# Optimization experiments

Hardware: AMD Instinct MI355X
Metric: run time of the kernel (lower is better)

## Reference

```python
import jax, jax.numpy as jnp
import numpy as np

N_NODES = 50000
N_EDGES = 800000
IN_CH = 256
OUT_CH = 64
HEADS = 4
NEG_SLOPE = 0.2


def setup_inputs() -> dict:
    key = jax.random.key(0)
    k = jax.random.split(key, 7)
    x = jax.random.normal(k[0], (N_NODES, IN_CH), dtype=jnp.float32)
    edge_index = jax.random.randint(k[1], (2, N_EDGES), 0, N_NODES, dtype=jnp.int32)
    # Glorot-style init for the linear projection and attention vectors
    W = jax.random.normal(k[2], (IN_CH, HEADS * OUT_CH), dtype=jnp.float32) / np.sqrt(IN_CH)
    att_src = jax.random.normal(k[3], (HEADS, OUT_CH), dtype=jnp.float32) / np.sqrt(OUT_CH)
    att_dst = jax.random.normal(k[4], (HEADS, OUT_CH), dtype=jnp.float32) / np.sqrt(OUT_CH)
    bias = jnp.zeros((HEADS * OUT_CH,), dtype=jnp.float32)
    return {"x": x, "edge_index": edge_index, "W": W,
            "att_src": att_src, "att_dst": att_dst, "bias": bias}


def reference(x, edge_index, W, att_src, att_dst, bias):
    N = x.shape[0]
    # PyG GATConv default: add self-loops
    loop = jnp.arange(N, dtype=edge_index.dtype)
    src = jnp.concatenate([edge_index[0], loop])
    dst = jnp.concatenate([edge_index[1], loop])

    h = (x @ W).reshape(N, HEADS, OUT_CH)          # [N,H,C]
    a_src = jnp.einsum('nhc,hc->nh', h, att_src)    # [N,H]
    a_dst = jnp.einsum('nhc,hc->nh', h, att_dst)    # [N,H]

    alpha = a_src[src] + a_dst[dst]                 # [E,H]
    alpha = jax.nn.leaky_relu(alpha, NEG_SLOPE)

    # segment softmax over edges grouped by destination node
    amax = jax.ops.segment_max(alpha, dst, num_segments=N)
    amax = jnp.where(jnp.isfinite(amax), amax, 0.0)
    e = jnp.exp(alpha - amax[dst])
    denom = jax.ops.segment_sum(e, dst, num_segments=N)
    coef = e / (denom[dst] + 1e-16)                 # [E,H]

    msg = coef[..., None] * h[src]                  # [E,H,C]
    out = jax.ops.segment_sum(msg, dst, num_segments=N)  # [N,H,C]
    out = out.reshape(N, HEADS * OUT_CH) + bias
    return jax.nn.relu(out)
```

## Files before the change

### kernel.cpp

```cpp
#include <hip/hip_runtime.h>
#include <hip/hip_bf16.h>

#define HC 256
#define NEG_SLOPE 0.2f
#define LDA 264

typedef short short8_t __attribute__((ext_vector_type(8)));
typedef float float4_t __attribute__((ext_vector_type(4)));

__device__ __forceinline__ unsigned short f2bf(float f) {
  unsigned u = __float_as_uint(f);
  return (unsigned short)((u + 0x7fffu + ((u >> 16) & 1u)) >> 16);
}
__device__ __forceinline__ float bf2f(unsigned short b) {
  return __uint_as_float(((unsigned)b) << 16);
}

__global__ void wt_deg(const float* __restrict__ W, unsigned short* __restrict__ Wt,
                       const int* __restrict__ ei, int* __restrict__ deg, int E)
{
  if (blockIdx.x < 256) {
    const int k = blockIdx.x;
    const int n = threadIdx.x;
    Wt[n * 256 + k] = f2bf(W[k * 256 + n]);
    return;
  }
  const int base = ((blockIdx.x - 256) * 256 + threadIdx.x) * 4;
  if (base + 3 < E) {
    const int4 d4 = *(const int4*)&ei[E + base];
    atomicAdd(&deg[d4.x], 1);
    atomicAdd(&deg[d4.y], 1);
    atomicAdd(&deg[d4.z], 1);
    atomicAdd(&deg[d4.w], 1);
  } else {
    for (int e = base; e < E; ++e) atomicAdd(&deg[ei[E + e]], 1);
  }
}

__global__ __launch_bounds__(256) void gemm_mfma(
    const float* __restrict__ x, const unsigned short* __restrict__ Wt,
    const float* __restrict__ att_src, const float* __restrict__ att_dst,
    unsigned short* __restrict__ h, float* __restrict__ a_src,
    float* __restrict__ a_dst, int nnodes)
{
  __shared__ unsigned short As[64 * LDA];
  const int t    = threadIdx.x;
  const int wv   = t >> 6;
  const int lane = t & 63;
  const int r0   = blockIdx.x * 64;

  {
    const int row = t >> 2;
    const int kc  = (t & 3) * 64;
    const int gr  = r0 + row;
    unsigned pk[32];
    if (gr < nnodes) {
      const float4* p = (const float4*)(x + (size_t)gr * 256 + kc);
      #pragma unroll
      for (int i = 0; i < 16; ++i) {
        const float4 v = p[i];
        __hip_bfloat162 b0 = __float22bfloat162_rn(make_float2(v.x, v.y));
        __hip_bfloat162 b1 = __float22bfloat162_rn(make_float2(v.z, v.w));
        pk[2 * i]     = *(unsigned*)&b0;
        pk[2 * i + 1] = *(unsigned*)&b1;
      }
    } else {
      #pragma unroll
      for (int i = 0; i < 32; ++i) pk[i] = 0;
    }
    uint4* d = (uint4*)&As[row * LDA + kc];
    #pragma unroll
    for (int i = 0; i < 8; ++i)
      d[i] = make_uint4(pk[4 * i], pk[4 * i + 1], pk[4 * i + 2], pk[4 * i + 3]);
  }
  __syncthreads();

  const int q = lane >> 4, l15 = lane & 15;
  float4_t acc[4][4] = {};

  #pragma unroll
  for (int ks = 0; ks < 8; ++ks) {
    const int ko = ks * 32 + q * 8;
    short8_t bfr[4], af[4];
    #pragma unroll
    for (int nt = 0; nt < 4; ++nt)
      bfr[nt] = *(const short8_t*)&Wt[(size_t)(64 * wv + 16 * nt + l15) * 256 + ko];
    #pragma unroll
    for (int mt = 0; mt < 4; ++mt)
      af[mt] = *(const short8_t*)&As[(16 * mt + l15) * LDA + ko];
    #pragma unroll
    for (int mt = 0; mt < 4; ++mt)
      #pragma unroll
      for (int nt = 0; nt < 4; ++nt)
        acc[mt][nt] = __builtin_amdgcn_mfma_f32_16x16x32_bf16(
            af[mt], bfr[nt], acc[mt][nt], 0, 0, 0);
  }

  float atts[4], attd[4];
  #pragma unroll
  for (int nt = 0; nt < 4; ++nt) {
    atts[nt] = att_src[wv * 64 + 16 * nt + l15];
    attd[nt] = att_dst[wv * 64 + 16 * nt + l15];
  }

  #pragma unroll
  for (int mt = 0; mt < 4; ++mt) {
    #pragma unroll
    for (int reg = 0; reg < 4; ++reg) {
      const int row = r0 + 16 * mt + 4 * q + reg;
      const bool ok = row < nnodes;
      float ps = 0.f, pd = 0.f;
      #pragma unroll
      for (int nt = 0; nt < 4; ++nt) {
        const float v = acc[mt][nt][reg];
        if (ok) h[(size_t)row * 256 + 64 * wv + 16 * nt + l15] = f2bf(v);
        ps += v * atts[nt];
        pd += v * attd[nt];
      }
      #pragma unroll
      for (int off = 8; off; off >>= 1) {
        ps += __shfl_down(ps, off, 16);
        pd += __shfl_down(pd, off, 16);
      }
      if (ok && l15 == 0) {
        a_src[row * 4 + wv] = ps;
        a_dst[row * 4 + wv] = pd;
      }
    }
  }
}

__global__ __launch_bounds__(256) void scan_p1(const int* __restrict__ deg,
                                               int* __restrict__ bsum, int n)
{
  __shared__ int ws[4];
  const int t = threadIdx.x, lane = t & 63, wv = t >> 6;
  const int base = blockIdx.x * 1024 + t * 4;
  int4 v = make_int4(0, 0, 0, 0);
  if (base + 3 < n) v = *(const int4*)&deg[base];
  else {
    if (base + 0 < n) v.x = deg[base + 0];
    if (base + 1 < n) v.y = deg[base + 1];
    if (base + 2 < n) v.z = deg[base + 2];
  }
  int s = (v.x + v.y) + (v.z + v.w);
  #pragma unroll
  for (int off = 32; off; off >>= 1) s += __shfl_down(s, off, 64);
  if (lane == 0) ws[wv] = s;
  __syncthreads();
  if (t == 0) bsum[blockIdx.x] = (ws[0] + ws[1]) + (ws[2] + ws[3]);
}

__global__ __launch_bounds__(1024) void scan_p2(const int* __restrict__ bsum,
                                                int* __restrict__ boff,
                                                int* __restrict__ rowptr,
                                                int nb, int n)
{
  __shared__ int wsum[16], woff[16];
  const int t = threadIdx.x, lane = t & 63, wv = t >> 6;
  int v = (t < nb) ? bsum[t] : 0;
  int sc = v;
  #pragma unroll
  for (int off = 1; off < 64; off <<= 1) {
    int u = __shfl_up(sc, off, 64);
    if (lane >= off) sc += u;
  }
  if (lane == 63) wsum[wv] = sc;
  __syncthreads();
  if (t == 0) {
    int run = 0;
    #pragma unroll
    for (int i = 0; i < 16; ++i) { int x = wsum[i]; woff[i] = run; run += x; }
    rowptr[n] = run;
  }
  __syncthreads();
  if (t < nb) boff[t] = woff[wv] + sc - v;
}

__global__ __launch_bounds__(256) void scan_p3(const int* __restrict__ deg,
                                               const int* __restrict__ boff,
                                               int* __restrict__ rowptr,
                                               int* __restrict__ cursor, int n)
{
  __shared__ int wsum[4], woff[4];
  const int t = threadIdx.x, lane = t & 63, wv = t >> 6;
  const int base = blockIdx.x * 1024 + t * 4;
  int4 v = make_int4(0, 0, 0, 0);
  if (base + 3 < n) v = *(const int4*)&deg[base];
  else {
    if (base + 0 < n) v.x = deg[base + 0];
    if (base + 1 < n) v.y = deg[base + 1];
    if (base + 2 < n) v.z = deg[base + 2];
  }
  const int s = (v.x + v.y) + (v.z + v.w);
  int sc = s;
  #pragma unroll
  for (int off = 1; off < 64; off <<= 1) {
    int u = __shfl_up(sc, off, 64);
    if (lane >= off) sc += u;
  }
  if (lane == 63) wsum[wv] = sc;
  __syncthreads();
  if (t == 0) {
    int run = 0;
    #pragma unroll
    for (int i = 0; i < 4; ++i) { int x = wsum[i]; woff[i] = run; run += x; }
  }
  __syncthreads();
  int excl = boff[blockIdx.x] + woff[wv] + (sc - s);
  int4 r;
  r.x = excl;
  r.y = r.x + v.x;
  r.z = r.y + v.y;
  r.w = r.z + v.z;
  if (base + 3 < n) {
    *(int4*)&rowptr[base] = r;
    *(int4*)&cursor[base] = r;
  } else {
    if (base + 0 < n) { rowptr[base + 0] = r.x; cursor[base + 0] = r.x; }
    if (base + 1 < n) { rowptr[base + 1] = r.y; cursor[base + 1] = r.y; }
    if (base + 2 < n) { rowptr[base + 2] = r.z; cursor[base + 2] = r.z; }
  }
}

__device__ __forceinline__ void fill_one(
    int s, int d, int dlo, int dhi, const float* __restrict__ a_src,
    const float* __restrict__ a_dst, int* __restrict__ cursor,
    int* __restrict__ csr_src, float4* __restrict__ wexp)
{
  if (d < dlo || d >= dhi) return;
  const int pos = atomicAdd(&cursor[d], 1);
  csr_src[pos] = s;
  const float4 as = ((const float4*)a_src)[s];
  const float4 ad = ((const float4*)a_dst)[d];
  float4 al;
  al.x = as.x + ad.x; al.y = as.y + ad.y;
  al.z = as.z + ad.z; al.w = as.w + ad.w;
  al.x = al.x > 0.f ? al.x : NEG_SLOPE * al.x;
  al.y = al.y > 0.f ? al.y : NEG_SLOPE * al.y;
  al.z = al.z > 0.f ? al.z : NEG_SLOPE * al.z;
  al.w = al.w > 0.f ? al.w : NEG_SLOPE * al.w;
  al.x = expf(al.x); al.y = expf(al.y); al.z = expf(al.z); al.w = expf(al.w);
  wexp[pos] = al;
}

__global__ __launch_bounds__(256) void fill_csr(
    const int* __restrict__ ei, const float* __restrict__ a_src,
    const float* __restrict__ a_dst, int* __restrict__ cursor,
    int* __restrict__ csr_src, float4* __restrict__ wexp, int E, int nnodes)
{
  const int g    = blockIdx.x & 7;
  const int bg   = blockIdx.x >> 3;
  const int nbg  = gridDim.x >> 3;
  const int gsz  = (nnodes + 7) >> 3;
  const int dlo  = g * gsz;
  const int dhi  = min(dlo + gsz, nnodes);
  const int E4   = E >> 2;

  for (int c = bg * 256 + threadIdx.x; c < E4; c += nbg * 256) {
    const int4 d4 = *(const int4*)&ei[E + 4 * c];
    const int4 s4 = *(const int4*)&ei[4 * c];
    fill_one(s4.x, d4.x, dlo, dhi, a_src, a_dst, cursor, csr_src, wexp);
    fill_one(s4.y, d4.y, dlo, dhi, a_src, a_dst, cursor, csr_src, wexp);
    fill_one(s4.z, d4.z, dlo, dhi, a_src, a_dst, cursor, csr_src, wexp);
    fill_one(s4.w, d4.w, dlo, dhi, a_src, a_dst, cursor, csr_src, wexp);
  }
  for (int e = E4 * 4 + bg * 256 + threadIdx.x; e < E; e += nbg * 256)
    fill_one(ei[e], ei[E + e], dlo, dhi, a_src, a_dst, cursor, csr_src, wexp);
}

__device__ __forceinline__ float4 ld_h(const unsigned short* __restrict__ h,
                                       int row, int cb)
{
  const ushort4 u = *(const ushort4*)&h[(size_t)row * 256 + cb];
  return make_float4(bf2f(u.x), bf2f(u.y), bf2f(u.z), bf2f(u.w));
}

__global__ __launch_bounds__(256) void gather_kernel(
    const int* __restrict__ rowptr, const int* __restrict__ csr_src,
    const float* __restrict__ wexp, const unsigned short* __restrict__ h,
    const float* __restrict__ a_src, const float* __restrict__ a_dst,
    const float* __restrict__ bias, float* __restrict__ out, int n)
{
  const int per8 = gridDim.x >> 3;
  const int vb   = (blockIdx.x & 7) * per8 + (blockIdx.x >> 3);
  const int wave = threadIdx.x >> 6;
  const int lane = threadIdx.x & 63;
  const int d = vb * 4 + wave;
  if (d >= n) return;

  const int head = lane >> 4;
  const int cb   = lane * 4;

  float alpha = a_src[d * 4 + head] + a_dst[d * 4 + head];
  alpha = alpha > 0.f ? alpha : NEG_SLOPE * alpha;
  float w = expf(alpha);
  float dsum = w;
  float4 hv = ld_h(h, d, cb);
  float4 acc = make_float4(w * hv.x, w * hv.y, w * hv.z, w * hv.w);

  int j = rowptr[d];
  const int end = rowptr[d + 1];

  for (; j + 7 < end; j += 8) {
    const int4 sa = *(const int4*)&csr_src[j];
    const int4 sb = *(const int4*)&csr_src[j + 4];
    float wj[8];
    #pragma unroll
    for (int k = 0; k < 8; ++k) wj[k] = wexp[(j + k) * 4 + head];
    const float4 h0 = ld_h(h, sa.x, cb);
    const float4 h1 = ld_h(h, sa.y, cb);
    const float4 h2 = ld_h(h, sa.z, cb);
    const float4 h3 = ld_h(h, sa.w, cb);
    const float4 h4 = ld_h(h, sb.x, cb);
    const float4 h5 = ld_h(h, sb.y, cb);
    const float4 h6 = ld_h(h, sb.z, cb);
    const float4 h7 = ld_h(h, sb.w, cb);
    dsum += ((wj[0] + wj[1]) + (wj[2] + wj[3])) + ((wj[4] + wj[5]) + (wj[6] + wj[7]));
    acc.x += wj[0] * h0.x + wj[1] * h1.x + wj[2] * h2.x + wj[3] * h3.x
           + wj[4] * h4.x + wj[5] * h5.x + wj[6] * h6.x + wj[7] * h7.x;
    acc.y += wj[0] * h0.y + wj[1] * h1.y + wj[2] * h2.y + wj[3] * h3.y
           + wj[4] * h4.y + wj[5] * h5.y + wj[6] * h6.y + wj[7] * h7.y;
    acc.z += wj[0] * h0.z + wj[1] * h1.z + wj[2] * h2.z + wj[3] * h3.z
           + wj[4] * h4.z + wj[5] * h5.z + wj[6] * h6.z + wj[7] * h7.z;
    acc.w += wj[0] * h0.w + wj[1] * h1.w + wj[2] * h2.w + wj[3] * h3.w
           + wj[4] * h4.w + wj[5] * h5.w + wj[6] * h6.w + wj[7] * h7.w;
  }
  for (; j < end; ++j) {
    const int s0 = csr_src[j];
    const float w0 = wexp[j * 4 + head];
    const float4 h0 = ld_h(h, s0, cb);
    dsum += w0;
    acc.x += w0 * h0.x; acc.y += w0 * h0.y;
    acc.z += w0 * h0.z; acc.w += w0 * h0.w;
  }

  const float inv = 1.f / (dsum + 1e-16f);
  const float4 b4 = ((const float4*)bias)[lane];
  float4 o;
  o.x = acc.x * inv + b4.x; o.x = o.x > 0.f ? o.x : 0.f;
  o.y = acc.y * inv + b4.y; o.y = o.y > 0.f ? o.y : 0.f;
  o.z = acc.z * inv + b4.z; o.z = o.z > 0.f ? o.z : 0.f;
  o.w = acc.w * inv + b4.w; o.w = o.w > 0.f ? o.w : 0.f;
  *(float4*)&out[(size_t)d * 256 + cb] = o;
}

extern "C" void kernel_launch(void* const* d_in, const int* in_sizes, int n_in,
                              void* d_out, int out_size, void* d_ws, size_t ws_size,
                              hipStream_t stream)
{
  const float* x       = (const float*)d_in[0];
  const int*   ei      = (const int*)d_in[1];
  const float* W       = (const float*)d_in[2];
  const float* att_src = (const float*)d_in[3];
  const float* att_dst = (const float*)d_in[4];
  const float* bias    = (const float*)d_in[5];

  const int nnodes = in_sizes[0] / HC;
  const int E      = in_sizes[1] / 2;
  const int nb     = (nnodes + 1023) / 1024;
  const int degBlocks    = (E + 1023) / 1024;
  const int gemmBlocks   = (nnodes + 63) / 64;
  const int gatherBlocks = (((nnodes + 3) / 4) + 7) & ~7;

  float* out = (float*)d_out;
  char* ws = (char*)d_ws;
  unsigned short* h  = (unsigned short*)ws;
  float* a_src = (float*)(ws + (size_t)nnodes * HC * 2);
  float* a_dst = a_src + (size_t)nnodes * 4;
  unsigned short* Wt = (unsigned short*)(a_dst + (size_t)nnodes * 4);
  int* deg    = (int*)((char*)Wt + 256 * 256 * 2);
  int* rowptr = deg + nnodes;
  int* cursor = rowptr + ((nnodes + 1 + 3) & ~3);
  int* bsum   = cursor + nnodes;
  int* boff   = bsum + ((nb + 3) & ~3);
  float4* wexp = (float4*)(boff + ((nb + 3) & ~3));
  int* csr    = (int*)(wexp + E);

  hipMemsetAsync(deg, 0, (size_t)nnodes * sizeof(int), stream);

  wt_deg<<<256 + degBlocks, 256, 0, stream>>>(W, Wt, ei, deg, E);

  gemm_mfma<<<gemmBlocks, 256, 0, stream>>>(
      x, Wt, att_src, att_dst, h, a_src, a_dst, nnodes);

  scan_p1<<<nb, 256, 0, stream>>>(deg, bsum, nnodes);
  scan_p2<<<1, 1024, 0, stream>>>(bsum, boff, rowptr, nb, nnodes);
  scan_p3<<<nb, 256, 0, stream>>>(deg, boff, rowptr, cursor, nnodes);

  fill_csr<<<1024, 256, 0, stream>>>(ei, a_src, a_dst, cursor, csr,
                                     (float4*)wexp, E, nnodes);

  gather_kernel<<<gatherBlocks, 256, 0, stream>>>(
      rowptr, csr, (const float*)wexp, h, a_src, a_dst, bias, out, nnodes);
}
```

Measured before the change: 282.7 us.

## Pack CSR source and bf16 edge weights into one record; transpose GEMM epilogue

Edge source index and the four exp-weights are now stored as one 16-byte record per CSR slot, with the weights held in bf16. The gather then does a single coalesced load per edge instead of separate csr and wexp loads, and fill_csr loads the source index only for edges in its destination range. The GEMM swaps its MFMA operands so each lane holds four consecutive columns, which allows packed 8-byte h stores and a shorter attention reduction using two xor shuffles. The cost is lower weight precision and a 4-byte pad per record.

```diff
diff --git a/kernel.cpp b/kernel.cpp
--- a/kernel.cpp
+++ b/kernel.cpp
@@ -14,6 +14,10 @@
 }
 __device__ __forceinline__ float bf2f(unsigned short b) {
   return __uint_as_float(((unsigned)b) << 16);
+}
+__device__ __forceinline__ unsigned pk2bf(float a, float b) {
+  __hip_bfloat162 b2 = __float22bfloat162_rn(make_float2(a, b));
+  return *(unsigned*)&b2;
 }
 
 __global__ void wt_deg(const float* __restrict__ W, unsigned short* __restrict__ Wt,
@@ -59,10 +63,8 @@
       #pragma unroll
       for (int i = 0; i < 16; ++i) {
         const float4 v = p[i];
-        __hip_bfloat162 b0 = __float22bfloat162_rn(make_float2(v.x, v.y));
-        __hip_bfloat162 b1 = __float22bfloat162_rn(make_float2(v.z, v.w));
-        pk[2 * i]     = *(unsigned*)&b0;
-        pk[2 * i + 1] = *(unsigned*)&b1;
+        pk[2 * i]     = pk2bf(v.x, v.y);
+        pk[2 * i + 1] = pk2bf(v.z, v.w);
       }
     } else {
       #pragma unroll
@@ -93,39 +95,36 @@
       #pragma unroll
       for (int nt = 0; nt < 4; ++nt)
         acc[mt][nt] = __builtin_amdgcn_mfma_f32_16x16x32_bf16(
-            af[mt], bfr[nt], acc[mt][nt], 0, 0, 0);
-  }
-
-  float atts[4], attd[4];
+            bfr[nt], af[mt], acc[mt][nt], 0, 0, 0);
+  }
+
+  float4 atts[4], attd[4];
   #pragma unroll
   for (int nt = 0; nt < 4; ++nt) {
-    atts[nt] = att_src[wv * 64 + 16 * nt + l15];
-    attd[nt] = att_dst[wv * 64 + 16 * nt + l15];
+    atts[nt] = ((const float4*)att_src)[16 * wv + 4 * nt + q];
+    attd[nt] = ((const float4*)att_dst)[16 * wv + 4 * nt + q];
   }
 
   #pragma unroll
   for (int mt = 0; mt < 4; ++mt) {
-    #pragma unroll
-    for (int reg = 0; reg < 4; ++reg) {
-      const int row = r0 + 16 * mt + 4 * q + reg;
-      const bool ok = row < nnodes;
-      float ps = 0.f, pd = 0.f;
-      #pragma unroll
-      for (int nt = 0; nt < 4; ++nt) {
-        const float v = acc[mt][nt][reg];
-        if (ok) h[(size_t)row * 256 + 64 * wv + 16 * nt + l15] = f2bf(v);
-        ps += v * atts[nt];
-        pd += v * attd[nt];
+    const int row = r0 + 16 * mt + l15;
+    const bool ok = row < nnodes;
+    float ps = 0.f, pd = 0.f;
+    #pragma unroll
+    for (int nt = 0; nt < 4; ++nt) {
+      const float4_t a = acc[mt][nt];
+      if (ok) {
+        uint2 u = make_uint2(pk2bf(a[0], a[1]), pk2bf(a[2], a[3]));
+        *(uint2*)&h[(size_t)row * 256 + 64 * wv + 16 * nt + 4 * q] = u;
       }
-      #pragma unroll
-      for (int off = 8; off; off >>= 1) {
-        ps += __shfl_down(ps, off, 16);
-        pd += __shfl_down(pd, off, 16);
-      }
-      if (ok && l15 == 0) {
-        a_src[row * 4 + wv] = ps;
-        a_dst[row * 4 + wv] = pd;
-      }
+      ps += a[0] * atts[nt].x + a[1] * atts[nt].y + a[2] * atts[nt].z + a[3] * atts[nt].w;
+      pd += a[0] * attd[nt].x + a[1] * attd[nt].y + a[2] * attd[nt].z + a[3] * attd[nt].w;
+    }
+    ps += __shfl_xor(ps, 16, 64); ps += __shfl_xor(ps, 32, 64);
+    pd += __shfl_xor(pd, 16, 64); pd += __shfl_xor(pd, 32, 64);
+    if (ok && q == 0) {
+      a_src[row * 4 + wv] = ps;
+      a_dst[row * 4 + wv] = pd;
     }
   }
 }
@@ -224,13 +223,13 @@
 }
 
 __device__ __forceinline__ void fill_one(
-    int s, int d, int dlo, int dhi, const float* __restrict__ a_src,
-    const float* __restrict__ a_dst, int* __restrict__ cursor,
-    int* __restrict__ csr_src, float4* __restrict__ wexp)
+    const int* __restrict__ ei, int e, int d, int dlo, int dhi,
+    const float* __restrict__ a_src, const float* __restrict__ a_dst,
+    int* __restrict__ cursor, uint4* __restrict__ rec)
 {
   if (d < dlo || d >= dhi) return;
+  const int s = ei[e];
   const int pos = atomicAdd(&cursor[d], 1);
-  csr_src[pos] = s;
   const float4 as = ((const float4*)a_src)[s];
   const float4 ad = ((const float4*)a_dst)[d];
   float4 al;
@@ -241,13 +240,13 @@
   al.z = al.z > 0.f ? al.z : NEG_SLOPE * al.z;
   al.w = al.w > 0.f ? al.w : NEG_SLOPE * al.w;
   al.x = expf(al.x); al.y = expf(al.y); al.z = expf(al.z); al.w = expf(al.w);
-  wexp[pos] = al;
+  rec[pos] = make_uint4((unsigned)s, pk2bf(al.x, al.y), pk2bf(al.z, al.w), 0u);
 }
 
 __global__ __launch_bounds__(256) void fill_csr(
     const int* __restrict__ ei, const float* __restrict__ a_src,
     const float* __restrict__ a_dst, int* __restrict__ cursor,
-    int* __restrict__ csr_src, float4* __restrict__ wexp, int E, int nnodes)
+    uint4* __restrict__ rec, int E, int nnodes)
 {
   const int g    = blockIdx.x & 7;
   const int bg   = blockIdx.x >> 3;
@@ -259,14 +258,13 @@
 
   for (int c = bg * 256 + threadIdx.x; c < E4; c += nbg * 256) {
     const int4 d4 = *(const int4*)&ei[E + 4 * c];
-    const int4 s4 = *(const int4*)&ei[4 * c];
-    fill_one(s4.x, d4.x, dlo, dhi, a_src, a_dst, cursor, csr_src, wexp);
-    fill_one(s4.y, d4.y, dlo, dhi, a_src, a_dst, cursor, csr_src, wexp);
-    fill_one(s4.z, d4.z, dlo, dhi, a_src, a_dst, cursor, csr_src, wexp);
-    fill_one(s4.w, d4.w, dlo, dhi, a_src, a_dst, cursor, csr_src, wexp);
+    fill_one(ei, 4 * c + 0, d4.x, dlo, dhi, a_src, a_dst, cursor, rec);
+    fill_one(ei, 4 * c + 1, d4.y, dlo, dhi, a_src, a_dst, cursor, rec);
+    fill_one(ei, 4 * c + 2, d4.z, dlo, dhi, a_src, a_dst, cursor, rec);
+    fill_one(ei, 4 * c + 3, d4.w, dlo, dhi, a_src, a_dst, cursor, rec);
   }
   for (int e = E4 * 4 + bg * 256 + threadIdx.x; e < E; e += nbg * 256)
-    fill_one(ei[e], ei[E + e], dlo, dhi, a_src, a_dst, cursor, csr_src, wexp);
+    fill_one(ei, e, ei[E + e], dlo, dhi, a_src, a_dst, cursor, rec);
 }
 
 __device__ __forceinline__ float4 ld_h(const unsigned short* __restrict__ h,
@@ -275,12 +273,18 @@
   const ushort4 u = *(const ushort4*)&h[(size_t)row * 256 + cb];
   return make_float4(bf2f(u.x), bf2f(u.y), bf2f(u.z), bf2f(u.w));
 }
+__device__ __forceinline__ float wsel(uint4 r, int head)
+{
+  const unsigned pw = (head & 2) ? r.z : r.y;
+  const unsigned us = (head & 1) ? (pw >> 16) : (pw & 0xffffu);
+  return __uint_as_float(us << 16);
+}
 
 __global__ __launch_bounds__(256) void gather_kernel(
-    const int* __restrict__ rowptr, const int* __restrict__ csr_src,
-    const float* __restrict__ wexp, const unsigned short* __restrict__ h,
-    const float* __restrict__ a_src, const float* __restrict__ a_dst,
-    const float* __restrict__ bias, float* __restrict__ out, int n)
+    const int* __restrict__ rowptr, const uint4* __restrict__ rec,
+    const unsigned short* __restrict__ h, const float* __restrict__ a_src,
+    const float* __restrict__ a_dst, const float* __restrict__ bias,
+    float* __restrict__ out, int n)
 {
   const int per8 = gridDim.x >> 3;
   const int vb   = (blockIdx.x & 7) * per8 + (blockIdx.x >> 3);
@@ -303,33 +307,45 @@
   const int end = rowptr[d + 1];
 
   for (; j + 7 < end; j += 8) {
-    const int4 sa = *(const int4*)&csr_src[j];
-    const int4 sb = *(const int4*)&csr_src[j + 4];
+    uint4 r[8];
+    #pragma unroll
+    for (int k = 0; k < 8; ++k) r[k] = rec[j + k];
+    float4 hx[8];
+    #pragma unroll
+    for (int k = 0; k < 8; ++k) hx[k] = ld_h(h, (int)r[k].x, cb);
     float wj[8];
     #pragma unroll
-    for (int k = 0; k < 8; ++k) wj[k] = wexp[(j + k) * 4 + head];
-    const float4 h0 = ld_h(h, sa.x, cb);
-    const float4 h1 = ld_h(h, sa.y, cb);
-    const float4 h2 = ld_h(h, sa.z, cb);
-    const float4 h3 = ld_h(h, sa.w, cb);
-    const float4 h4 = ld_h(h, sb.x, cb);
-    const float4 h5 = ld_h(h, sb.y, cb);
-    const float4 h6 = ld_h(h, sb.z, cb);
-    const float4 h7 = ld_h(h, sb.w, cb);
+    for (int k = 0; k < 8; ++k) wj[k] = wsel(r[k], head);
     dsum += ((wj[0] + wj[1]) + (wj[2] + wj[3])) + ((wj[4] + wj[5]) + (wj[6] + wj[7]));
-    acc.x += wj[0] * h0.x + wj[1] * h1.x + wj[2] * h2.x + wj[3] * h3.x
-           + wj[4] * h4.x + wj[5] * h5.x + wj[6] * h6.x + wj[7] * h7.x;
-    acc.y += wj[0] * h0.y + wj[1] * h1.y + wj[2] * h2.y + wj[3] * h3.y
-           + wj[4] * h4.y + wj[5] * h5.y + wj[6] * h6.y + wj[7] * h7.y;
-    acc.z += wj[0] * h0.z + wj[1] * h1.z + wj[2] * h2.z + wj[3] * h3.z
-           + wj[4] * h4.z + wj[5] * h5.z + wj[6] * h6.z + wj[7] * h7.z;
-    acc.w += wj[0] * h0.w + wj[1] * h1.w + wj[2] * h2.w + wj[3] * h3.w
-           + wj[4] * h4.w + wj[5] * h5.w + wj[6] * h6.w + wj[7] * h7.w;
+    #pragma unroll
+    for (int k = 0; k < 8; ++k) {
+      acc.x += wj[k] * hx[k].x;
+      acc.y += wj[k] * hx[k].y;
+      acc.z += wj[k] * hx[k].z;
+      acc.w += wj[k] * hx[k].w;
+    }
+  }
+  for (; j + 3 < end; j += 4) {
+    uint4 r[4];
+    #pragma unroll
+    for (int k = 0; k < 4; ++k) r[k] = rec[j + k];
+    float4 hx[4];
+    #pragma unroll
+    for (int k = 0; k < 4; ++k) hx[k] = ld_h(h, (int)r[k].x, cb);
+    #pragma unroll
+    for (int k = 0; k < 4; ++k) {
+      const float wk = wsel(r[k], head);
+      dsum += wk;
+      acc.x += wk * hx[k].x;
+      acc.y += wk * hx[k].y;
+      acc.z += wk * hx[k].z;
+      acc.w += wk * hx[k].w;
+    }
   }
   for (; j < end; ++j) {
-    const int s0 = csr_src[j];
-    const float w0 = wexp[j * 4 + head];
-    const float4 h0 = ld_h(h, s0, cb);
+    const uint4 r0 = rec[j];
+    const float4 h0 = ld_h(h, (int)r0.x, cb);
+    const float w0 = wsel(r0, head);
     dsum += w0;
     acc.x += w0 * h0.x; acc.y += w0 * h0.y;
     acc.z += w0 * h0.z; acc.w += w0 * h0.w;
@@ -374,8 +390,7 @@
   int* cursor = rowptr + ((nnodes + 1 + 3) & ~3);
   int* bsum   = cursor + nnodes;
   int* boff   = bsum + ((nb + 3) & ~3);
-  float4* wexp = (float4*)(boff + ((nb + 3) & ~3));
-  int* csr    = (int*)(wexp + E);
+  uint4* rec  = (uint4*)(boff + ((nb + 3) & ~3));
 
   hipMemsetAsync(deg, 0, (size_t)nnodes * sizeof(int), stream);
 
@@ -388,9 +403,8 @@
   scan_p2<<<1, 1024, 0, stream>>>(bsum, boff, rowptr, nb, nnodes);
   scan_p3<<<nb, 256, 0, stream>>>(deg, boff, rowptr, cursor, nnodes);
 
-  fill_csr<<<1024, 256, 0, stream>>>(ei, a_src, a_dst, cursor, csr,
-                                     (float4*)wexp, E, nnodes);
+  fill_csr<<<1024, 256, 0, stream>>>(ei, a_src, a_dst, cursor, rec, E, nnodes);
 
   gather_kernel<<<gatherBlocks, 256, 0, stream>>>(
-      rowptr, csr, (const float*)wexp, h, a_src, a_dst, bias, out, nnodes);
-}
+      rowptr, rec, h, a_src, a_dst, bias, out, nnodes);
+}
```

Result: no change. 279.6 us (-1.1%).
